# Performance work log

Measured on AMD Instinct MI355X. Metric: run time of the kernel, lower is better.

The kernel has to match this reference:

```python
import jax, jax.numpy as jnp
import numpy as np

EPS = 1e-8


def setup_inputs() -> dict:
    key = jax.random.key(0)
    k1, k2, k3, k4 = jax.random.split(key, 4)
    B, N, M, C = 512, 512, 128, 1024
    addr = M + 6  # read head: k(M) + beta(1) + g(1) + s(3) + gamma(1)
    controller_out = jax.random.normal(k1, (B, C), dtype=jnp.float32)
    prev_w = jax.random.uniform(k2, (B, N), dtype=jnp.float32)
    prev_w = prev_w / prev_w.sum(axis=1, keepdims=True)  # valid weighting
    memory_state = jax.random.normal(k3, (B, N, M), dtype=jnp.float32)
    W_fc = jax.random.normal(k4, (C, addr), dtype=jnp.float32) * 0.02
    b_fc = jnp.zeros((addr,), dtype=jnp.float32)
    return {"controller_out": controller_out, "prev_w": prev_w,
            "memory_state": memory_state, "W_fc": W_fc, "b_fc": b_fc}


def reference(controller_out, prev_w, memory_state, W_fc, b_fc):
    M = memory_state.shape[2]
    out = controller_out @ W_fc + b_fc  # [B, M+6]
    k = out[:, :M]                                   # key
    beta = jax.nn.softplus(out[:, M:M + 1])          # key strength
    g = jax.nn.sigmoid(out[:, M + 1:M + 2])          # interpolation gate
    s = jax.nn.softmax(out[:, M + 2:M + 5], axis=1)  # 3-tap shift weights
    gamma = 1.0 + jax.nn.softplus(out[:, M + 5:M + 6])

    # Content addressing (Eq. 5-6): cosine similarity + sharpened softmax
    norm_k = jnp.linalg.norm(k, axis=1, keepdims=True) + EPS      # [B,1]
    norm_mem = jnp.linalg.norm(memory_state, axis=2) + EPS        # [B,N]
    sim = jnp.einsum('bnm,bm->bn', memory_state, k) / (norm_k * norm_mem)
    w_c = jax.nn.softmax(beta * sim, axis=1)

    # Interpolation (Eq. 7)
    w_g = g * w_c + (1.0 - g) * prev_w

    # Circular 3-tap shift (Eq. 8): vectorized roll instead of per-slot loop
    w_s = (s[:, 0:1] * jnp.roll(w_g, 1, axis=1)
           + s[:, 1:2] * w_g
           + s[:, 2:3] * jnp.roll(w_g, -1, axis=1))

    # Sharpening (Eq. 9)
    w_pow = w_s ** gamma
    w = w_pow / (w_pow.sum(axis=1, keepdims=True) + EPS)

    # Read vector (read head)
    read_vec = jnp.einsum('bn,bnm->bm', w, memory_state)
    return (read_vec, w)
```

## Files before the change

### kernel.cpp

```cpp
#include <hip/hip_runtime.h>
#include <math.h>

#define BB   512
#define NN   512
#define MM   128
#define CC   1024
#define ADDR 134
#define EPSF 1e-8f
#define WSSTRIDE 136

__device__ __forceinline__ float softplus_f(float x) {
    return fmaxf(x, 0.0f) + log1pf(expf(-fabsf(x)));
}

__global__ __launch_bounds__(192) void ntm_fc_kernel(
    const float* __restrict__ co,
    const float* __restrict__ W_fc,
    const float* __restrict__ b_fc,
    float* __restrict__ ws)
{
    __shared__ __align__(16) float s_co[2 * CC];
    __shared__ float s_nr[2][2];
    __shared__ float s_ex[2][8];

    const int t = threadIdx.x;
    const int b0 = blockIdx.x * 2;

    {
        const float4* src = (const float4*)(co + (size_t)b0 * CC);
        float4* dst = (float4*)s_co;
        for (int i = t; i < 512; i += 192) dst[i] = src[i];
    }
    __syncthreads();

    float k0 = 0.f, k1 = 0.f;
    if (t < ADDR) {
        float a00 = 0.f, a01 = 0.f, a10 = 0.f, a11 = 0.f;
        const float* Wj = W_fc + t;
        for (int c = 0; c < CC; c += 8) {
            float wv[8];
            #pragma unroll
            for (int i = 0; i < 8; ++i) wv[i] = Wj[(size_t)(c + i) * ADDR];
            #pragma unroll
            for (int i = 0; i < 8; ++i) {
                if (i & 1) { a01 = fmaf(wv[i], s_co[c + i], a01);
                             a11 = fmaf(wv[i], s_co[CC + c + i], a11); }
                else       { a00 = fmaf(wv[i], s_co[c + i], a00);
                             a10 = fmaf(wv[i], s_co[CC + c + i], a10); }
            }
        }
        float bias = b_fc[t];
        k0 = a00 + a01 + bias;
        k1 = a10 + a11 + bias;
        if (t >= MM) { s_ex[0][t - MM] = k0; s_ex[1][t - MM] = k1; }
        else {
            ws[(size_t)b0 * WSSTRIDE + t] = k0;
            ws[(size_t)(b0 + 1) * WSSTRIDE + t] = k1;
        }
    }
    if (t < MM) {
        float v0 = k0 * k0, v1 = k1 * k1;
        #pragma unroll
        for (int off = 32; off >= 1; off >>= 1) {
            v0 += __shfl_xor(v0, off, 64);
            v1 += __shfl_xor(v1, off, 64);
        }
        if ((t & 63) == 0) { s_nr[t >> 6][0] = v0; s_nr[t >> 6][1] = v1; }
    }
    __syncthreads();
    if (t < 2) {
        float ks = s_nr[0][t] + s_nr[1][t];
        float norm_k = sqrtf(ks) + EPSF;
        float beta = softplus_f(s_ex[t][0]);
        float g = 1.0f / (1.0f + expf(-s_ex[t][1]));
        float e0 = s_ex[t][2], e1 = s_ex[t][3], e2 = s_ex[t][4];
        float mx = fmaxf(e0, fmaxf(e1, e2));
        float x0 = expf(e0 - mx), x1 = expf(e1 - mx), x2 = expf(e2 - mx);
        float inv = 1.0f / (x0 + x1 + x2);
        float* p = ws + (size_t)(b0 + t) * WSSTRIDE + MM;
        p[0] = beta / norm_k;
        p[1] = g;
        p[2] = x0 * inv;
        p[3] = x1 * inv;
        p[4] = x2 * inv;
        p[5] = 1.0f + softplus_f(s_ex[t][5]);
    }
}

__global__ __launch_bounds__(1024) void ntm_main_kernel(
    const float* __restrict__ prev_w,
    const float* __restrict__ mem,
    const float* __restrict__ ws,
    float* __restrict__ out_rv,
    float* __restrict__ out_w)
{
    __shared__ __align__(16) float s_k[MM];
    __shared__ float s_params[8];
    __shared__ float s_bsim[NN];
    __shared__ float s_wg[NN];
    __shared__ float s_w[NN];
    __shared__ __align__(16) float s_part[32 * MM];
    __shared__ float s_redA[16];
    __shared__ float s_redB[16];

    const int t = threadIdx.x;
    const int b = blockIdx.x;
    const int wv = t >> 6;

    float pw = (t < NN) ? prev_w[(size_t)b * NN + t] : 0.0f;

    if (t < WSSTRIDE) {
        float v = ws[(size_t)b * WSSTRIDE + t];
        if (t < MM) s_k[t] = v; else s_params[t - MM] = v;
    }
    __syncthreads();

    const float bnk = s_params[0];
    const float4* memb = (const float4*)(mem + (size_t)b * NN * MM);

    {
        const int l4 = t & 3;
        const int row0 = t >> 2;
        float4 kf[8];
        #pragma unroll
        for (int i = 0; i < 8; ++i) kf[i] = ((const float4*)s_k)[l4 + 4 * i];

        float maxv = -INFINITY;
        #pragma unroll
        for (int it = 0; it < 2; ++it) {
            const int row = row0 + it * 256;
            const float4* rp = memb + (size_t)row * 32;
            float4 a[8];
            #pragma unroll
            for (int i = 0; i < 8; ++i) a[i] = rp[l4 + 4 * i];
            float d = 0.f, q = 0.f;
            #pragma unroll
            for (int i = 0; i < 8; ++i) {
                d = fmaf(a[i].x, kf[i].x, d); q = fmaf(a[i].x, a[i].x, q);
                d = fmaf(a[i].y, kf[i].y, d); q = fmaf(a[i].y, a[i].y, q);
                d = fmaf(a[i].z, kf[i].z, d); q = fmaf(a[i].z, a[i].z, q);
                d = fmaf(a[i].w, kf[i].w, d); q = fmaf(a[i].w, a[i].w, q);
            }
            d += __shfl_xor(d, 1, 64); q += __shfl_xor(q, 1, 64);
            d += __shfl_xor(d, 2, 64); q += __shfl_xor(q, 2, 64);
            float bsim = bnk * d / (sqrtf(q) + EPSF);
            maxv = fmaxf(maxv, bsim);
            if (l4 == 0) s_bsim[row] = bsim;
        }
        #pragma unroll
        for (int off = 32; off >= 1; off >>= 1) maxv = fmaxf(maxv, __shfl_xor(maxv, off, 64));
        if ((t & 63) == 0) s_redA[wv] = maxv;
    }
    __syncthreads();

    float Mx = -INFINITY;
    #pragma unroll
    for (int i = 0; i < 16; ++i) Mx = fmaxf(Mx, s_redA[i]);

    {
        const bool act = (t < NN);
        float e = act ? expf(s_bsim[t] - Mx) : 0.0f;
        float ls = e;
        #pragma unroll
        for (int off = 32; off >= 1; off >>= 1) ls += __shfl_xor(ls, off, 64);
        if ((t & 63) == 0) s_redB[wv] = ls;
        __syncthreads();
        float S = 0.f;
        #pragma unroll
        for (int i = 0; i < 16; ++i) S += s_redB[i];

        const float invS = 1.0f / S;
        const float g = s_params[1];
        float wg = 0.0f;
        if (act) { wg = fmaf(g, e * invS, (1.0f - g) * pw); s_wg[t] = wg; }
        __syncthreads();

        float wp = 0.0f;
        if (act) {
            float wsv = s_params[2] * s_wg[(t + NN - 1) & (NN - 1)]
                      + s_params[3] * wg
                      + s_params[4] * s_wg[(t + 1) & (NN - 1)];
            wp = powf(wsv, s_params[5]);
        }
        float lz = wp;
        #pragma unroll
        for (int off = 32; off >= 1; off >>= 1) lz += __shfl_xor(lz, off, 64);
        if ((t & 63) == 0) s_redA[wv] = lz;
        __syncthreads();
        float Z = 0.f;
        #pragma unroll
        for (int i = 0; i < 16; ++i) Z += s_redA[i];

        if (act) {
            float w = wp / (Z + EPSF);
            s_w[t] = w;
            out_w[(size_t)b * NN + t] = w;
        }
    }
    __syncthreads();

    {
        const int q = t >> 5;
        const int l = t & 31;
        float4 acc = make_float4(0.f, 0.f, 0.f, 0.f);
        const int nb = q * 16;
        #pragma unroll
        for (int i = 0; i < 16; i += 4) {
            const int n = nb + i;
            float4 a0 = memb[(size_t)(n    ) * 32 + l];
            float4 a1 = memb[(size_t)(n + 1) * 32 + l];
            float4 a2 = memb[(size_t)(n + 2) * 32 + l];
            float4 a3 = memb[(size_t)(n + 3) * 32 + l];
            float w0 = s_w[n], w1 = s_w[n + 1], w2 = s_w[n + 2], w3 = s_w[n + 3];
            acc.x = fmaf(w0, a0.x, acc.x); acc.y = fmaf(w0, a0.y, acc.y);
            acc.z = fmaf(w0, a0.z, acc.z); acc.w = fmaf(w0, a0.w, acc.w);
            acc.x = fmaf(w1, a1.x, acc.x); acc.y = fmaf(w1, a1.y, acc.y);
            acc.z = fmaf(w1, a1.z, acc.z); acc.w = fmaf(w1, a1.w, acc.w);
            acc.x = fmaf(w2, a2.x, acc.x); acc.y = fmaf(w2, a2.y, acc.y);
            acc.z = fmaf(w2, a2.z, acc.z); acc.w = fmaf(w2, a2.w, acc.w);
            acc.x = fmaf(w3, a3.x, acc.x); acc.y = fmaf(w3, a3.y, acc.y);
            acc.z = fmaf(w3, a3.z, acc.z); acc.w = fmaf(w3, a3.w, acc.w);
        }
        *((float4*)&s_part[q * MM + l * 4]) = acc;
        __syncthreads();
        if (t < MM) {
            float r = 0.f;
            #pragma unroll
            for (int q2 = 0; q2 < 32; ++q2) r += s_part[q2 * MM + t];
            out_rv[(size_t)b * MM + t] = r;
        }
    }
}

extern "C" void kernel_launch(void* const* d_in, const int* in_sizes, int n_in,
                              void* d_out, int out_size, void* d_ws, size_t ws_size,
                              hipStream_t stream) {
    const float* co     = (const float*)d_in[0];
    const float* prev_w = (const float*)d_in[1];
    const float* mem    = (const float*)d_in[2];
    const float* W_fc   = (const float*)d_in[3];
    const float* b_fc   = (const float*)d_in[4];
    float* out = (float*)d_out;
    float* ws  = (float*)d_ws;

    ntm_fc_kernel<<<BB / 2, 192, 0, stream>>>(co, W_fc, b_fc, ws);
    ntm_main_kernel<<<BB, 1024, 0, stream>>>(prev_w, mem, ws,
                                             out, out + (size_t)BB * MM);
}
```

Before: 258.0 us.

## Split main kernel into multi-block similarity pass and separate read pass

The single 1024-thread-per-batch kernel is replaced by two kernels. A similarity kernel uses four 256-thread blocks per batch row; each computes the exponentiated cosine scores and a partial sum and writes them to the workspace. A 512-thread read kernel then does interpolation, shift, sharpening and the weighted read. This spreads the memory-bound similarity phase over more blocks and drops the max-subtraction step, but it reads memory_state a second time in a separate launch, where it is less likely to still be in cache. It also adds a launch and relies on exp not overflowing, since beta times a cosine in [-1,1] is unbounded.

```diff
diff --git a/kernel.cpp b/kernel.cpp
--- a/kernel.cpp
+++ b/kernel.cpp
@@ -8,6 +8,8 @@
 #define ADDR 134
 #define EPSF 1e-8f
 #define WSSTRIDE 136
+#define EOFF  131072
+#define POFF  (EOFF + BB * NN)
 
 __device__ __forceinline__ float softplus_f(float x) {
     return fmaxf(x, 0.0f) + log1pf(expf(-fabsf(x)));
@@ -87,131 +89,122 @@
     }
 }
 
-__global__ __launch_bounds__(1024) void ntm_main_kernel(
+__global__ __launch_bounds__(256) void ntm_sim_kernel(
+    const float* __restrict__ mem,
+    float* __restrict__ ws)
+{
+    __shared__ __align__(16) float s_k[MM];
+    __shared__ float s_red[4];
+    __shared__ float s_bnk;
+
+    const int t = threadIdx.x;
+    const int bid = blockIdx.x;
+    const int b = bid >> 2;
+    const int rc = bid & 3;
+
+    if (t < MM) s_k[t] = ws[(size_t)b * WSSTRIDE + t];
+    if (t == MM) s_bnk = ws[(size_t)b * WSSTRIDE + MM];
+    __syncthreads();
+
+    const int l4 = t & 3;
+    const int r  = t >> 2;
+    float4 kf[8];
+    #pragma unroll
+    for (int i = 0; i < 8; ++i) kf[i] = ((const float4*)s_k)[l4 + 4 * i];
+    const float bnk = s_bnk;
+    const float4* memb = (const float4*)(mem + (size_t)b * NN * MM);
+
+    float esum = 0.f;
+    #pragma unroll
+    for (int it = 0; it < 2; ++it) {
+        const int row = rc * 128 + it * 64 + r;
+        const float4* rp = memb + (size_t)row * 32;
+        float4 a[8];
+        #pragma unroll
+        for (int i = 0; i < 8; ++i) a[i] = rp[l4 + 4 * i];
+        float d = 0.f, q = 0.f;
+        #pragma unroll
+        for (int i = 0; i < 8; ++i) {
+            d = fmaf(a[i].x, kf[i].x, d); q = fmaf(a[i].x, a[i].x, q);
+            d = fmaf(a[i].y, kf[i].y, d); q = fmaf(a[i].y, a[i].y, q);
+            d = fmaf(a[i].z, kf[i].z, d); q = fmaf(a[i].z, a[i].z, q);
+            d = fmaf(a[i].w, kf[i].w, d); q = fmaf(a[i].w, a[i].w, q);
+        }
+        d += __shfl_xor(d, 1, 64); q += __shfl_xor(q, 1, 64);
+        d += __shfl_xor(d, 2, 64); q += __shfl_xor(q, 2, 64);
+        float e = expf(bnk * d / (sqrtf(q) + EPSF));
+        if (l4 == 0) {
+            ws[EOFF + (size_t)b * NN + row] = e;
+            esum += e;
+        }
+    }
+    #pragma unroll
+    for (int off = 32; off >= 1; off >>= 1) esum += __shfl_xor(esum, off, 64);
+    if ((t & 63) == 0) s_red[t >> 6] = esum;
+    __syncthreads();
+    if (t == 0)
+        ws[POFF + bid] = s_red[0] + s_red[1] + s_red[2] + s_red[3];
+}
+
+__global__ __launch_bounds__(512) void ntm_read_kernel(
     const float* __restrict__ prev_w,
     const float* __restrict__ mem,
     const float* __restrict__ ws,
     float* __restrict__ out_rv,
     float* __restrict__ out_w)
 {
-    __shared__ __align__(16) float s_k[MM];
     __shared__ float s_params[8];
-    __shared__ float s_bsim[NN];
     __shared__ float s_wg[NN];
     __shared__ float s_w[NN];
-    __shared__ __align__(16) float s_part[32 * MM];
-    __shared__ float s_redA[16];
-    __shared__ float s_redB[16];
+    __shared__ float s_red[8];
+    __shared__ __align__(16) float s_part[16 * MM];
 
     const int t = threadIdx.x;
     const int b = blockIdx.x;
-    const int wv = t >> 6;
-
-    float pw = (t < NN) ? prev_w[(size_t)b * NN + t] : 0.0f;
-
-    if (t < WSSTRIDE) {
-        float v = ws[(size_t)b * WSSTRIDE + t];
-        if (t < MM) s_k[t] = v; else s_params[t - MM] = v;
-    }
-    __syncthreads();
-
-    const float bnk = s_params[0];
-    const float4* memb = (const float4*)(mem + (size_t)b * NN * MM);
+
+    float pw = prev_w[(size_t)b * NN + t];
+    float e  = ws[EOFF + (size_t)b * NN + t];
+    float S  = ws[POFF + b * 4 + 0] + ws[POFF + b * 4 + 1]
+             + ws[POFF + b * 4 + 2] + ws[POFF + b * 4 + 3];
+    if (t < 6) s_params[t] = ws[(size_t)b * WSSTRIDE + MM + t];
+    __syncthreads();
+
+    const float g = s_params[1];
+    float wg = fmaf(g, e / S, (1.0f - g) * pw);
+    s_wg[t] = wg;
+    __syncthreads();
+
+    float wsv = s_params[2] * s_wg[(t + NN - 1) & (NN - 1)]
+              + s_params[3] * wg
+              + s_params[4] * s_wg[(t + 1) & (NN - 1)];
+    float wp = powf(wsv, s_params[5]);
+
+    float lz = wp;
+    #pragma unroll
+    for (int off = 32; off >= 1; off >>= 1) lz += __shfl_xor(lz, off, 64);
+    if ((t & 63) == 0) s_red[t >> 6] = lz;
+    __syncthreads();
+    float Z = 0.f;
+    #pragma unroll
+    for (int i = 0; i < 8; ++i) Z += s_red[i];
+
+    float w = wp / (Z + EPSF);
+    out_w[(size_t)b * NN + t] = w;
+    s_w[t] = w;
+    __syncthreads();
 
     {
-        const int l4 = t & 3;
-        const int row0 = t >> 2;
-        float4 kf[8];
-        #pragma unroll
-        for (int i = 0; i < 8; ++i) kf[i] = ((const float4*)s_k)[l4 + 4 * i];
-
-        float maxv = -INFINITY;
-        #pragma unroll
-        for (int it = 0; it < 2; ++it) {
-            const int row = row0 + it * 256;
-            const float4* rp = memb + (size_t)row * 32;
-            float4 a[8];
-            #pragma unroll
-            for (int i = 0; i < 8; ++i) a[i] = rp[l4 + 4 * i];
-            float d = 0.f, q = 0.f;
-            #pragma unroll
-            for (int i = 0; i < 8; ++i) {
-                d = fmaf(a[i].x, kf[i].x, d); q = fmaf(a[i].x, a[i].x, q);
-                d = fmaf(a[i].y, kf[i].y, d); q = fmaf(a[i].y, a[i].y, q);
-                d = fmaf(a[i].z, kf[i].z, d); q = fmaf(a[i].z, a[i].z, q);
-                d = fmaf(a[i].w, kf[i].w, d); q = fmaf(a[i].w, a[i].w, q);
-            }
-            d += __shfl_xor(d, 1, 64); q += __shfl_xor(q, 1, 64);
-            d += __shfl_xor(d, 2, 64); q += __shfl_xor(q, 2, 64);
-            float bsim = bnk * d / (sqrtf(q) + EPSF);
-            maxv = fmaxf(maxv, bsim);
-            if (l4 == 0) s_bsim[row] = bsim;
-        }
-        #pragma unroll
-        for (int off = 32; off >= 1; off >>= 1) maxv = fmaxf(maxv, __shfl_xor(maxv, off, 64));
-        if ((t & 63) == 0) s_redA[wv] = maxv;
-    }
-    __syncthreads();
-
-    float Mx = -INFINITY;
-    #pragma unroll
-    for (int i = 0; i < 16; ++i) Mx = fmaxf(Mx, s_redA[i]);
-
-    {
-        const bool act = (t < NN);
-        float e = act ? expf(s_bsim[t] - Mx) : 0.0f;
-        float ls = e;
-        #pragma unroll
-        for (int off = 32; off >= 1; off >>= 1) ls += __shfl_xor(ls, off, 64);
-        if ((t & 63) == 0) s_redB[wv] = ls;
-        __syncthreads();
-        float S = 0.f;
-        #pragma unroll
-        for (int i = 0; i < 16; ++i) S += s_redB[i];
-
-        const float invS = 1.0f / S;
-        const float g = s_params[1];
-        float wg = 0.0f;
-        if (act) { wg = fmaf(g, e * invS, (1.0f - g) * pw); s_wg[t] = wg; }
-        __syncthreads();
-
-        float wp = 0.0f;
-        if (act) {
-            float wsv = s_params[2] * s_wg[(t + NN - 1) & (NN - 1)]
-                      + s_params[3] * wg
-                      + s_params[4] * s_wg[(t + 1) & (NN - 1)];
-            wp = powf(wsv, s_params[5]);
-        }
-        float lz = wp;
-        #pragma unroll
-        for (int off = 32; off >= 1; off >>= 1) lz += __shfl_xor(lz, off, 64);
-        if ((t & 63) == 0) s_redA[wv] = lz;
-        __syncthreads();
-        float Z = 0.f;
-        #pragma unroll
-        for (int i = 0; i < 16; ++i) Z += s_redA[i];
-
-        if (act) {
-            float w = wp / (Z + EPSF);
-            s_w[t] = w;
-            out_w[(size_t)b * NN + t] = w;
-        }
-    }
-    __syncthreads();
-
-    {
-        const int q = t >> 5;
-        const int l = t & 31;
+        const int gp = t >> 5;
+        const int l  = t & 31;
+        const float4* memb = (const float4*)(mem + (size_t)b * NN * MM);
         float4 acc = make_float4(0.f, 0.f, 0.f, 0.f);
-        const int nb = q * 16;
-        #pragma unroll
-        for (int i = 0; i < 16; i += 4) {
-            const int n = nb + i;
-            float4 a0 = memb[(size_t)(n    ) * 32 + l];
-            float4 a1 = memb[(size_t)(n + 1) * 32 + l];
-            float4 a2 = memb[(size_t)(n + 2) * 32 + l];
-            float4 a3 = memb[(size_t)(n + 3) * 32 + l];
-            float w0 = s_w[n], w1 = s_w[n + 1], w2 = s_w[n + 2], w3 = s_w[n + 3];
+        for (int kk = 0; kk < 32; kk += 4) {
+            const int r0 = gp + 16 * kk;
+            float4 a0 = memb[(size_t)(r0      ) * 32 + l];
+            float4 a1 = memb[(size_t)(r0 + 16 ) * 32 + l];
+            float4 a2 = memb[(size_t)(r0 + 32 ) * 32 + l];
+            float4 a3 = memb[(size_t)(r0 + 48 ) * 32 + l];
+            float w0 = s_w[r0], w1 = s_w[r0 + 16], w2 = s_w[r0 + 32], w3 = s_w[r0 + 48];
             acc.x = fmaf(w0, a0.x, acc.x); acc.y = fmaf(w0, a0.y, acc.y);
             acc.z = fmaf(w0, a0.z, acc.z); acc.w = fmaf(w0, a0.w, acc.w);
             acc.x = fmaf(w1, a1.x, acc.x); acc.y = fmaf(w1, a1.y, acc.y);
@@ -221,12 +214,12 @@
             acc.x = fmaf(w3, a3.x, acc.x); acc.y = fmaf(w3, a3.y, acc.y);
             acc.z = fmaf(w3, a3.z, acc.z); acc.w = fmaf(w3, a3.w, acc.w);
         }
-        *((float4*)&s_part[q * MM + l * 4]) = acc;
+        *((float4*)&s_part[gp * MM + l * 4]) = acc;
         __syncthreads();
         if (t < MM) {
             float r = 0.f;
             #pragma unroll
-            for (int q2 = 0; q2 < 32; ++q2) r += s_part[q2 * MM + t];
+            for (int q2 = 0; q2 < 16; ++q2) r += s_part[q2 * MM + t];
             out_rv[(size_t)b * MM + t] = r;
         }
     }
@@ -244,6 +237,7 @@
     float* ws  = (float*)d_ws;
 
     ntm_fc_kernel<<<BB / 2, 192, 0, stream>>>(co, W_fc, b_fc, ws);
-    ntm_main_kernel<<<BB, 1024, 0, stream>>>(prev_w, mem, ws,
-                                             out, out + (size_t)BB * MM);
-}
+    ntm_sim_kernel<<<BB * 4, 256, 0, stream>>>(mem, ws);
+    ntm_read_kernel<<<BB, 512, 0, stream>>>(prev_w, mem, ws,
+                                            out, out + (size_t)BB * MM);
+}
```

New measurement: 264.6 us. 1.03x slower.
